# Performance work log

Measured on AMD Instinct MI355X. Metric: run time of the kernel, lower is better.

Reference implementation:

```python
import jax, jax.numpy as jnp
import numpy as np

D_MODEL = 1024
N_HEADS = 16
HEAD_DIM = 64
T = 4096
ROT = HEAD_DIM // 2          # 32 channels get rotary
PAIR = ROT // 2              # 16 cos/sin frequencies
EPS = 1e-6
SCALE = 0.12                 # constant attention scale (not 1/sqrt(d))
ROPE_BASE = 10000.0
VOCAB = 50257


def setup_inputs() -> dict:
    key = jax.random.key(0)
    k_x, k_qkv, k_o, k_tok = jax.random.split(key, 4)
    bound = 0.5 / np.sqrt(D_MODEL)
    x = jax.random.normal(k_x, (1, T, D_MODEL), dtype=jnp.float32)
    w_qkv = jax.random.uniform(k_qkv, (3 * D_MODEL, D_MODEL), jnp.float32, -bound, bound)
    # module uses zero_init for w_o; use small random so output is non-trivial
    w_o = jax.random.uniform(k_o, (D_MODEL, D_MODEL), jnp.float32, -bound, bound)
    q_norm_w = jnp.ones((HEAD_DIM,), jnp.float32)
    k_norm_w = jnp.ones((HEAD_DIM,), jnp.float32)
    tokens = jax.random.randint(k_tok, (1, T), 0, VOCAB, dtype=jnp.int64)
    pos = jnp.arange(T, dtype=jnp.int64)
    # RotaryCache: inv_freq over pair dims, cos/sin of t * inv_freq
    inv_freq = 1.0 / (ROPE_BASE ** (jnp.arange(PAIR, dtype=jnp.float32) / PAIR))
    freqs = jnp.arange(T, dtype=jnp.float32)[:, None] * inv_freq[None, :]  # [T, PAIR]
    return {
        "x": x, "tokens": tokens, "pos": pos,
        "w_qkv": w_qkv, "w_o": w_o,
        "q_norm_w": q_norm_w, "k_norm_w": k_norm_w,
        "cos": jnp.cos(freqs), "sin": jnp.sin(freqs),
        "window_tokens": 1024, "block_size": 128,
    }


def _rmsnorm(x, w):
    var = jnp.mean(x * x, axis=-1, keepdims=True)
    return x * jax.lax.rsqrt(var + EPS) * w


def reference(x, tokens, pos, w_qkv, w_o, q_norm_w, k_norm_w, cos, sin,
              window_tokens, block_size):
    B, Tq, C = x.shape
    H, Dh = N_HEADS, HEAD_DIM
    qkv = x @ w_qkv.T                                  # [B, T, 3C]
    q, k, v = jnp.split(qkv, 3, axis=-1)

    def to_bhtd(t):
        return t.reshape(B, Tq, H, Dh).transpose(0, 2, 1, 3)
    q, k, v = to_bhtd(q), to_bhtd(k), to_bhtd(v)

    q = _rmsnorm(q, q_norm_w)
    k = _rmsnorm(k, k_norm_w)

    # half-truncated RoPE: rotate first ROT channels pairwise (even/odd)
    c = cos[pos][None, None]                           # [1,1,T,PAIR]
    s = sin[pos][None, None]

    def rope_rotate(t):
        t1, t2 = t[..., :ROT], t[..., ROT:]
        even, odd = t1[..., 0::2], t1[..., 1::2]
        r_even = even * c - odd * s
        r_odd = even * s + odd * c
        t1r = jnp.stack([r_even, r_odd], axis=-1).reshape(t1.shape)
        return jnp.concatenate([t1r, t2], axis=-1)

    q = rope_rotate(q)
    k = rope_rotate(k)

    v = v * 0.5                                        # no value-embed branch

    scores = jnp.einsum('bhtd,bhsd->bhts', q, k) * SCALE
    idx = jnp.arange(Tq)
    diff = idx[:, None] - idx[None, :]
    allowed = (diff >= 0) & (diff < window_tokens)     # sliding causal window
    scores = jnp.where(allowed, scores, -jnp.inf)
    p = jax.nn.softmax(scores, axis=-1)
    out = jnp.einsum('bhts,bhsd->bhtd', p, v)
    out = out.transpose(0, 2, 1, 3).reshape(B, Tq, C)
    return out @ w_o.T
```

## Files before the change

### kernel.cpp

```cpp
#include <hip/hip_runtime.h>


typedef __bf16 bf16x8 __attribute__((ext_vector_type(8)));
typedef __bf16 bf16x2 __attribute__((ext_vector_type(2)));
typedef float f32x4 __attribute__((ext_vector_type(4)));
typedef unsigned short u16x8 __attribute__((ext_vector_type(8)));
typedef unsigned short u16x4 __attribute__((ext_vector_type(4)));

#define MFMA16(a, b, c) __builtin_amdgcn_mfma_f32_16x16x32_bf16((a), (b), (c), 0, 0, 0)

__device__ __forceinline__ unsigned short f2bf(float f) {
    unsigned int u = __float_as_uint(f);
    u += 0x7fffu + ((u >> 16) & 1u);
    return (unsigned short)(u >> 16);
}
__device__ __forceinline__ float bf2f(unsigned short h) {
    return __uint_as_float(((unsigned int)h) << 16);
}
__device__ __forceinline__ unsigned int pk2bf(float a, float b) {
#if __has_builtin(__builtin_amdgcn_cvt_pk_bf16_f32)
    bf16x2 v = __builtin_amdgcn_cvt_pk_bf16_f32(a, b);
    return __builtin_bit_cast(unsigned int, v);
#else
    return (unsigned int)f2bf(a) | ((unsigned int)f2bf(b) << 16);
#endif
}
__device__ __forceinline__ float fexp2(float x) {
#if __has_builtin(__builtin_amdgcn_exp2f)
    return __builtin_amdgcn_exp2f(x);
#else
    return exp2f(x);
#endif
}

__device__ __forceinline__ void gl_lds16(const void* g, void* l) {
    typedef __attribute__((address_space(1))) unsigned int GU;
    typedef __attribute__((address_space(3))) unsigned int LU;
    __builtin_amdgcn_global_load_lds((GU*)(unsigned long long)g,
                                     (LU*)(unsigned int)(unsigned long long)l,
                                     16, 0, 0);
}

__global__ void cvt3_kernel(const float* __restrict__ x,
                            const float* __restrict__ wqkv,
                            const float* __restrict__ wo,
                            unsigned short* __restrict__ xb,
                            unsigned short* __restrict__ wqkvb,
                            unsigned short* __restrict__ wob) {
    int i = blockIdx.x * 256 + threadIdx.x;
    const float* src;
    unsigned short* dst;
    int off;
    if (i < 1048576) { src = x; dst = xb; off = i; }
    else if (i < 1835008) { src = wqkv; dst = wqkvb; off = i - 1048576; }
    else { src = wo; dst = wob; off = i - 1835008; }
    float4 f = ((const float4*)src)[off];
    u16x4 o;
    o[0] = f2bf(f.x); o[1] = f2bf(f.y); o[2] = f2bf(f.z); o[3] = f2bf(f.w);
    ((u16x4*)dst)[off] = o;
}

#define TBS 72
__global__ __launch_bounds__(256, 3) void gemm_qkv(
    const unsigned short* __restrict__ A,
    const unsigned short* __restrict__ Bt,
    const float* __restrict__ cosb, const float* __restrict__ sinb,
    const float* __restrict__ qw, const float* __restrict__ kw,
    unsigned short* __restrict__ Qb,
    unsigned short* __restrict__ Kb,
    unsigned short* __restrict__ Vt)
{
    __shared__ unsigned short smem[16384];
    unsigned short* As0 = smem;
    unsigned short* As1 = smem + 4096;
    unsigned short* Bs0 = smem + 8192;
    unsigned short* Bs1 = smem + 12288;

    const int tid = threadIdx.x;
    const int wave = tid >> 6, lane = tid & 63;
    const int quad = lane >> 4, l16 = lane & 15;
    const int m0 = blockIdx.x * 128, n0 = blockIdx.y * 128;
    const int wm = (wave >> 1) * 64, wn = (wave & 1) * 64;

    f32x4 acc[4][4];
#pragma unroll
    for (int i = 0; i < 4; ++i)
#pragma unroll
        for (int j = 0; j < 4; ++j) acc[i][j] = (f32x4){0.f, 0.f, 0.f, 0.f};

    const int lrow = lane >> 2;
    const int lcol = ((lane & 3) ^ ((lane >> 3) & 3)) * 8;
    const int csw  = (quad ^ ((l16 >> 1) & 3)) * 8;

    for (int k0 = 0; k0 < 1024; k0 += 64) {
        {
            const unsigned short* ab = A + (size_t)(m0 + wave * 16 + lrow) * 1024 + k0 + lcol;
            gl_lds16(ab,              &As0[wave * 512]);
            gl_lds16(ab + 32,         &As1[wave * 512]);
            gl_lds16(ab + 65536,      &As0[2048 + wave * 512]);
            gl_lds16(ab + 65536 + 32, &As1[2048 + wave * 512]);
            const unsigned short* bb = Bt + (size_t)(n0 + wave * 16 + lrow) * 1024 + k0 + lcol;
            gl_lds16(bb,              &Bs0[wave * 512]);
            gl_lds16(bb + 32,         &Bs1[wave * 512]);
            gl_lds16(bb + 65536,      &Bs0[2048 + wave * 512]);
            gl_lds16(bb + 65536 + 32, &Bs1[2048 + wave * 512]);
        }
        __syncthreads();
        {
            bf16x8 af[4], bfr[4];
#pragma unroll
            for (int mt = 0; mt < 4; ++mt)
                af[mt] = *(const bf16x8*)&As0[(wm + mt * 16 + l16) * 32 + csw];
#pragma unroll
            for (int nt = 0; nt < 4; ++nt)
                bfr[nt] = *(const bf16x8*)&Bs0[(wn + nt * 16 + l16) * 32 + csw];
#pragma unroll
            for (int mt = 0; mt < 4; ++mt)
#pragma unroll
                for (int nt = 0; nt < 4; ++nt)
                    acc[mt][nt] = MFMA16(af[mt], bfr[nt], acc[mt][nt]);
        }
        {
            bf16x8 af[4], bfr[4];
#pragma unroll
            for (int mt = 0; mt < 4; ++mt)
                af[mt] = *(const bf16x8*)&As1[(wm + mt * 16 + l16) * 32 + csw];
#pragma unroll
            for (int nt = 0; nt < 4; ++nt)
                bfr[nt] = *(const bf16x8*)&Bs1[(wn + nt * 16 + l16) * 32 + csw];
#pragma unroll
            for (int mt = 0; mt < 4; ++mt)
#pragma unroll
                for (int nt = 0; nt < 4; ++nt)
                    acc[mt][nt] = MFMA16(af[mt], bfr[nt], acc[mt][nt]);
        }
        __syncthreads();
    }

    unsigned short* tbw = smem + wave * 1152;
    const int region = blockIdx.y >> 3;
    const int h = ((blockIdx.y & 7) << 1) + (wave & 1);

    if (region < 2) {
        const float* wgt = region ? kw : qw;
        unsigned short* dst = region ? Kb : Qb;
        const float post = region ? 1.f : 0.17312340490667046f;
        float w[4];
#pragma unroll
        for (int nt = 0; nt < 4; ++nt) w[nt] = wgt[nt * 16 + l16] * post;
#pragma unroll
        for (int mt = 0; mt < 4; ++mt) {
#pragma unroll
            for (int r = 0; r < 4; ++r) {
                const int row = m0 + wm + mt * 16 + quad * 4 + r;
                float ss = 0.f;
#pragma unroll
                for (int nt = 0; nt < 4; ++nt)
                    ss += acc[mt][nt][r] * acc[mt][nt][r];
                ss += __shfl_xor(ss, 1); ss += __shfl_xor(ss, 2);
                ss += __shfl_xor(ss, 4); ss += __shfl_xor(ss, 8);
                const float rn = rsqrtf(ss * (1.f / 64.f) + 1e-6f);
                float val[4];
#pragma unroll
                for (int nt = 0; nt < 4; ++nt)
                    val[nt] = acc[mt][nt][r] * rn * w[nt];
#pragma unroll
                for (int nt = 0; nt < 2; ++nt) {
                    const float prt = __shfl_xor(val[nt], 1);
                    const int p = nt * 8 + (l16 >> 1);
                    const float c = cosb[row * 16 + p];
                    const float s = sinb[row * 16 + p];
                    val[nt] = (l16 & 1) ? (prt * s + val[nt] * c)
                                        : (val[nt] * c - prt * s);
                }
#pragma unroll
                for (int nt = 0; nt < 4; ++nt)
                    tbw[(quad * 4 + r) * TBS + nt * 16 + l16] = f2bf(val[nt]);
            }
            const int t = lane >> 2, dcol = (lane & 3) * 16;
            u16x8 v0 = *(const u16x8*)&tbw[t * TBS + dcol];
            u16x8 v1 = *(const u16x8*)&tbw[t * TBS + dcol + 8];
            const size_t ob = ((size_t)h * 4096 + (m0 + wm + mt * 16 + t)) * 64 + dcol;
            *(u16x8*)&dst[ob] = v0;
            *(u16x8*)&dst[ob + 8] = v1;
        }
    } else {
#pragma unroll
        for (int mt = 0; mt < 4; ++mt) {
#pragma unroll
            for (int nt = 0; nt < 4; ++nt)
#pragma unroll
                for (int r = 0; r < 4; ++r)
                    tbw[(nt * 16 + l16) * 16 + quad * 4 + r] =
                        f2bf(acc[mt][nt][r] * 0.5f);
            u16x8 v0 = *(const u16x8*)&tbw[lane * 16];
            u16x8 v1 = *(const u16x8*)&tbw[lane * 16 + 8];
            const size_t vo = ((size_t)h * 64 + lane) * 4096 + m0 + wm + mt * 16;
            *(u16x8*)&Vt[vo] = v0;
            *(u16x8*)&Vt[vo + 8] = v1;
        }
    }
}

#define PSTR 72

template <int MASK>
__device__ __forceinline__ void attn_compute(
    int s0, int tq, int quad, int l16, int csw,
    const unsigned short* Ks0, const unsigned short* Ks1,
    const unsigned short* Vs0, const unsigned short* Vs1,
    unsigned short* Pw, const bf16x8 qf0, const bf16x8 qf1,
    f32x4 (&o)[4], float& lsum)
{
#pragma unroll
    for (int i = 0; i < 4; ++i) {
        const bf16x8 kf0 = *(const bf16x8*)&Ks0[(i * 16 + l16) * 32 + csw];
        const bf16x8 kf1 = *(const bf16x8*)&Ks1[(i * 16 + l16) * 32 + csw];
        f32x4 z = (f32x4){0.f, 0.f, 0.f, 0.f};
        z = MFMA16(kf0, qf0, z);
        z = MFMA16(kf1, qf1, z);
        float p[4];
#pragma unroll
        for (int r = 0; r < 4; ++r) {
            float e = fexp2(z[r]);
            if (MASK) {
                const int s = s0 + i * 16 + quad * 4 + r;
                e = ((unsigned)(tq - s) < 1024u) ? e : 0.f;
            }
            p[r] = e;
            lsum += e;
        }
        uint2 pk;
        pk.x = pk2bf(p[0], p[1]);
        pk.y = pk2bf(p[2], p[3]);
        *(uint2*)&Pw[l16 * PSTR + i * 16 + quad * 4] = pk;
    }
    const bf16x8 pf0 = *(const bf16x8*)&Pw[l16 * PSTR + quad * 8];
    const bf16x8 pf1 = *(const bf16x8*)&Pw[l16 * PSTR + 32 + quad * 8];
#pragma unroll
    for (int dt = 0; dt < 4; ++dt) {
        const bf16x8 vf0 = *(const bf16x8*)&Vs0[(dt * 16 + l16) * 32 + csw];
        const bf16x8 vf1 = *(const bf16x8*)&Vs1[(dt * 16 + l16) * 32 + csw];
        o[dt] = MFMA16(pf0, vf0, o[dt]);
        o[dt] = MFMA16(pf1, vf1, o[dt]);
    }
}

__global__ __launch_bounds__(512, 4) void attn_kernel(
    const unsigned short* __restrict__ Qb,
    const unsigned short* __restrict__ Kb,
    const unsigned short* __restrict__ Vt,
    unsigned short* __restrict__ att)
{
    __shared__ unsigned short Ks0[2][2048], Ks1[2][2048];
    __shared__ unsigned short Vs0[2][2048], Vs1[2][2048];
    __shared__ unsigned short P[8][16 * PSTR];

    const int bid = blockIdx.x;
    const int h = ((bid & 7) << 1) | ((bid >> 3) & 1);
    const int t0 = (31 - (bid >> 4)) * 128;

    const int tid = threadIdx.x;
    const int wave = tid >> 6, lane = tid & 63;
    const int quad = lane >> 4, l16 = lane & 15;
    const int qt0 = t0 + wave * 16;
    const int tq = qt0 + l16;
    const int srow = (tid & 255) >> 2;
    const int scol = ((tid & 3) ^ ((tid >> 3) & 3)) * 8;
    const int csw  = (quad ^ ((l16 >> 1) & 3)) * 8;

    const unsigned short* Qh = Qb + (size_t)h * 4096 * 64;
    const unsigned short* Kh = Kb + (size_t)h * 4096 * 64;
    const unsigned short* Vh = Vt + (size_t)h * 64 * 4096;

    const bf16x8 qf0 = *(const bf16x8*)&Qh[(qt0 + l16) * 64 + quad * 8];
    const bf16x8 qf1 = *(const bf16x8*)&Qh[(qt0 + l16) * 64 + 32 + quad * 8];

    f32x4 o[4];
#pragma unroll
    for (int dt = 0; dt < 4; ++dt) o[dt] = (f32x4){0.f, 0.f, 0.f, 0.f};
    float lsum = 0.f;
    unsigned short* Pw = P[wave];

    auto stage = [&](int b, int s0) {
        if (wave < 4) {
            const unsigned short* kb = Kh + (size_t)(s0 + srow) * 64 + scol;
            gl_lds16(kb,      &Ks0[b][wave * 512]);
            gl_lds16(kb + 32, &Ks1[b][wave * 512]);
        } else {
            const unsigned short* vb = Vh + (size_t)srow * 4096 + s0 + scol;
            gl_lds16(vb,      &Vs0[b][(wave - 4) * 512]);
            gl_lds16(vb + 32, &Vs1[b][(wave - 4) * 512]);
        }
    };

    const int s_lo = (t0 >= 1024) ? (t0 - 1024) : 0;
    const int s_hi = t0 + 64;
    stage(0, s_lo);
    __syncthreads();
    int buf = 0;
    for (int s0 = s_lo; s0 <= s_hi; s0 += 64) {
        if (s0 < s_hi) stage(buf ^ 1, s0 + 64);
        const bool dead = (s0 > qt0 + 15) || (s0 + 63 < qt0 - 1023);
        if (!dead) {
            const bool clean = (s0 + 63 <= qt0) && (s0 >= qt0 - 1008);
            if (clean)
                attn_compute<0>(s0, tq, quad, l16, csw, Ks0[buf], Ks1[buf],
                                Vs0[buf], Vs1[buf], Pw, qf0, qf1, o, lsum);
            else
                attn_compute<1>(s0, tq, quad, l16, csw, Ks0[buf], Ks1[buf],
                                Vs0[buf], Vs1[buf], Pw, qf0, qf1, o, lsum);
        }
        __syncthreads();
        buf ^= 1;
    }

    lsum += __shfl_xor(lsum, 16);
    lsum += __shfl_xor(lsum, 32);
    float lr[4];
#pragma unroll
    for (int r = 0; r < 4; ++r) lr[r] = 1.f / __shfl(lsum, quad * 4 + r);
#pragma unroll
    for (int dt = 0; dt < 4; ++dt)
#pragma unroll
        for (int r = 0; r < 4; ++r)
            att[(size_t)(qt0 + quad * 4 + r) * 1024 + h * 64 + dt * 16 + l16] =
                f2bf(o[dt][r] * lr[r]);
}

__global__ __launch_bounds__(256) void gemm_out(
    const unsigned short* __restrict__ A,
    const unsigned short* __restrict__ Bt,
    float* __restrict__ C)
{
    __shared__ unsigned short As0[2][2048], As1[2][2048];
    __shared__ unsigned short Bs0[2][4096], Bs1[2][4096];
    const int tid = threadIdx.x;
    const int wave = tid >> 6, lane = tid & 63;
    const int quad = lane >> 4, l16 = lane & 15;
    const int m0 = blockIdx.x * 64, n0 = blockIdx.y * 128;
    const int wm = (wave >> 1) * 32, wn = (wave & 1) * 64;
    const int lrow = lane >> 2;
    const int lcol = ((lane & 3) ^ ((lane >> 3) & 3)) * 8;
    const int csw  = (quad ^ ((l16 >> 1) & 3)) * 8;

    f32x4 acc[2][4];
#pragma unroll
    for (int i = 0; i < 2; ++i)
#pragma unroll
        for (int j = 0; j < 4; ++j) acc[i][j] = (f32x4){0.f, 0.f, 0.f, 0.f};

    auto stage = [&](int buf, int k0) {
        const unsigned short* ab = A + (size_t)(m0 + wave * 16 + lrow) * 1024 + k0 + lcol;
        gl_lds16(ab,      &As0[buf][wave * 512]);
        gl_lds16(ab + 32, &As1[buf][wave * 512]);
#pragma unroll
        for (int i = 0; i < 2; ++i) {
            const int c = wave * 2 + i;
            const unsigned short* bb = Bt + (size_t)(n0 + c * 16 + lrow) * 1024 + k0 + lcol;
            gl_lds16(bb,      &Bs0[buf][c * 512]);
            gl_lds16(bb + 32, &Bs1[buf][c * 512]);
        }
    };

    stage(0, 0);
    __syncthreads();
    int buf = 0;
    for (int k0 = 0; k0 < 1024; k0 += 64) {
        if (k0 + 64 < 1024) stage(buf ^ 1, k0 + 64);
        {
            bf16x8 af[2], bfr[4];
#pragma unroll
            for (int mt = 0; mt < 2; ++mt)
                af[mt] = *(const bf16x8*)&As0[buf][(wm + mt * 16 + l16) * 32 + csw];
#pragma unroll
            for (int nt = 0; nt < 4; ++nt)
                bfr[nt] = *(const bf16x8*)&Bs0[buf][(wn + nt * 16 + l16) * 32 + csw];
#pragma unroll
            for (int mt = 0; mt < 2; ++mt)
#pragma unroll
                for (int nt = 0; nt < 4; ++nt)
                    acc[mt][nt] = MFMA16(af[mt], bfr[nt], acc[mt][nt]);
        }
        {
            bf16x8 af[2], bfr[4];
#pragma unroll
            for (int mt = 0; mt < 2; ++mt)
                af[mt] = *(const bf16x8*)&As1[buf][(wm + mt * 16 + l16) * 32 + csw];
#pragma unroll
            for (int nt = 0; nt < 4; ++nt)
                bfr[nt] = *(const bf16x8*)&Bs1[buf][(wn + nt * 16 + l16) * 32 + csw];
#pragma unroll
            for (int mt = 0; mt < 2; ++mt)
#pragma unroll
                for (int nt = 0; nt < 4; ++nt)
                    acc[mt][nt] = MFMA16(af[mt], bfr[nt], acc[mt][nt]);
        }
        __syncthreads();
        buf ^= 1;
    }
#pragma unroll
    for (int mt = 0; mt < 2; ++mt)
#pragma unroll
        for (int nt = 0; nt < 4; ++nt)
#pragma unroll
            for (int r = 0; r < 4; ++r) {
                const int row = m0 + wm + mt * 16 + quad * 4 + r;
                const int col = n0 + wn + nt * 16 + l16;
                C[(size_t)row * 1024 + col] = acc[mt][nt][r];
            }
}

extern "C" void kernel_launch(void* const* d_in, const int* in_sizes, int n_in,
                              void* d_out, int out_size, void* d_ws, size_t ws_size,
                              hipStream_t stream) {
    const float* x    = (const float*)d_in[0];
    const float* wqkv = (const float*)d_in[3];
    const float* wo   = (const float*)d_in[4];
    const float* qw   = (const float*)d_in[5];
    const float* kw   = (const float*)d_in[6];
    const float* cosb = (const float*)d_in[7];
    const float* sinb = (const float*)d_in[8];

    char* ws = (char*)d_ws;
    if (ws_size < (size_t)48 * 1024 * 1024) return;
    unsigned short* xb    = (unsigned short*)(ws + ((size_t)0 << 20));
    unsigned short* wqkvb = (unsigned short*)(ws + ((size_t)8 << 20));
    unsigned short* wob   = (unsigned short*)(ws + ((size_t)14 << 20));
    unsigned short* Qb    = (unsigned short*)(ws + ((size_t)16 << 20));
    unsigned short* Kb    = (unsigned short*)(ws + ((size_t)24 << 20));
    unsigned short* Vt    = (unsigned short*)(ws + ((size_t)32 << 20));
    unsigned short* attb  = (unsigned short*)(ws + ((size_t)40 << 20));

    cvt3_kernel<<<8192, 256, 0, stream>>>(x, wqkv, wo, xb, wqkvb, wob);

    gemm_qkv<<<dim3(32, 24), 256, 0, stream>>>(xb, wqkvb, cosb, sinb, qw, kw,
                                               Qb, Kb, Vt);

    attn_kernel<<<512, 512, 0, stream>>>(Qb, Kb, Vt, attb);

    gemm_out<<<dim3(64, 8), 256, 0, stream>>>(attb, wob, (float*)d_out);
}
```

Before: 177.9 us.

## Restructure attention loop into 128-key tiles with split K/V staging and setprio

The attention main loop now processes 128 keys per iteration as two 64-key halves. K tiles are double-buffered one iteration ahead, while V is single-buffered and loaded within the same iteration, overlapping with the first QK/exp pass before a mid-iteration barrier. The PV MFMA section is wrapped in s_setprio to favour matrix issue. This halves the number of loop iterations and barriers per key, but V load latency is now exposed inside each iteration and LDS use goes up.

```diff
diff --git a/kernel.cpp b/kernel.cpp
--- a/kernel.cpp
+++ b/kernel.cpp
@@ -205,17 +205,15 @@
 #define PSTR 72
 
 template <int MASK>
-__device__ __forceinline__ void attn_compute(
-    int s0, int tq, int quad, int l16, int csw,
-    const unsigned short* Ks0, const unsigned short* Ks1,
-    const unsigned short* Vs0, const unsigned short* Vs1,
-    unsigned short* Pw, const bf16x8 qf0, const bf16x8 qf1,
-    f32x4 (&o)[4], float& lsum)
+__device__ __forceinline__ void qk_exp(
+    int sb, int tq, int quad, int l16, int csw, int rbase,
+    const unsigned short* KsA, const unsigned short* KsB,
+    unsigned short* Pw, const bf16x8 qf0, const bf16x8 qf1, float& lsum)
 {
 #pragma unroll
     for (int i = 0; i < 4; ++i) {
-        const bf16x8 kf0 = *(const bf16x8*)&Ks0[(i * 16 + l16) * 32 + csw];
-        const bf16x8 kf1 = *(const bf16x8*)&Ks1[(i * 16 + l16) * 32 + csw];
+        const bf16x8 kf0 = *(const bf16x8*)&KsA[(rbase + i * 16 + l16) * 32 + csw];
+        const bf16x8 kf1 = *(const bf16x8*)&KsB[(rbase + i * 16 + l16) * 32 + csw];
         f32x4 z = (f32x4){0.f, 0.f, 0.f, 0.f};
         z = MFMA16(kf0, qf0, z);
         z = MFMA16(kf1, qf1, z);
@@ -224,7 +222,7 @@
         for (int r = 0; r < 4; ++r) {
             float e = fexp2(z[r]);
             if (MASK) {
-                const int s = s0 + i * 16 + quad * 4 + r;
+                const int s = sb + i * 16 + quad * 4 + r;
                 e = ((unsigned)(tq - s) < 1024u) ? e : 0.f;
             }
             p[r] = e;
@@ -235,15 +233,24 @@
         pk.y = pk2bf(p[2], p[3]);
         *(uint2*)&Pw[l16 * PSTR + i * 16 + quad * 4] = pk;
     }
+}
+
+__device__ __forceinline__ void pv_acc(
+    int quad, int l16, int csw,
+    const unsigned short* VsA, const unsigned short* VsB,
+    const unsigned short* Pw, f32x4 (&o)[4])
+{
     const bf16x8 pf0 = *(const bf16x8*)&Pw[l16 * PSTR + quad * 8];
     const bf16x8 pf1 = *(const bf16x8*)&Pw[l16 * PSTR + 32 + quad * 8];
+    __builtin_amdgcn_s_setprio(1);
 #pragma unroll
     for (int dt = 0; dt < 4; ++dt) {
-        const bf16x8 vf0 = *(const bf16x8*)&Vs0[(dt * 16 + l16) * 32 + csw];
-        const bf16x8 vf1 = *(const bf16x8*)&Vs1[(dt * 16 + l16) * 32 + csw];
+        const bf16x8 vf0 = *(const bf16x8*)&VsA[(dt * 16 + l16) * 32 + csw];
+        const bf16x8 vf1 = *(const bf16x8*)&VsB[(dt * 16 + l16) * 32 + csw];
         o[dt] = MFMA16(pf0, vf0, o[dt]);
         o[dt] = MFMA16(pf1, vf1, o[dt]);
     }
+    __builtin_amdgcn_s_setprio(0);
 }
 
 __global__ __launch_bounds__(512, 4) void attn_kernel(
@@ -252,8 +259,9 @@
     const unsigned short* __restrict__ Vt,
     unsigned short* __restrict__ att)
 {
-    __shared__ unsigned short Ks0[2][2048], Ks1[2][2048];
-    __shared__ unsigned short Vs0[2][2048], Vs1[2][2048];
+    __shared__ unsigned short KsA[2][4096], KsB[2][4096];
+    __shared__ unsigned short Vs0[2048], Vs1[2048];
+    __shared__ unsigned short Vs2[2048], Vs3[2048];
     __shared__ unsigned short P[8][16 * PSTR];
 
     const int bid = blockIdx.x;
@@ -282,34 +290,54 @@
     float lsum = 0.f;
     unsigned short* Pw = P[wave];
 
-    auto stage = [&](int b, int s0) {
+    auto stageK = [&](int b, int s) {
         if (wave < 4) {
-            const unsigned short* kb = Kh + (size_t)(s0 + srow) * 64 + scol;
-            gl_lds16(kb,      &Ks0[b][wave * 512]);
-            gl_lds16(kb + 32, &Ks1[b][wave * 512]);
-        } else {
-            const unsigned short* vb = Vh + (size_t)srow * 4096 + s0 + scol;
-            gl_lds16(vb,      &Vs0[b][(wave - 4) * 512]);
-            gl_lds16(vb + 32, &Vs1[b][(wave - 4) * 512]);
+            const unsigned short* kb = Kh + (size_t)(s + srow) * 64 + scol;
+            gl_lds16(kb,             &KsA[b][wave * 512]);
+            gl_lds16(kb + 32,        &KsB[b][wave * 512]);
+            gl_lds16(kb + 4096,      &KsA[b][2048 + wave * 512]);
+            gl_lds16(kb + 4096 + 32, &KsB[b][2048 + wave * 512]);
         }
     };
+    auto stageV = [&](int s) {
+        if (wave >= 4) {
+            const unsigned short* vb = Vh + (size_t)srow * 4096 + s + scol;
+            gl_lds16(vb,      &Vs0[(wave - 4) * 512]);
+            gl_lds16(vb + 32, &Vs1[(wave - 4) * 512]);
+            gl_lds16(vb + 64, &Vs2[(wave - 4) * 512]);
+            gl_lds16(vb + 96, &Vs3[(wave - 4) * 512]);
+        }
+    };
 
     const int s_lo = (t0 >= 1024) ? (t0 - 1024) : 0;
-    const int s_hi = t0 + 64;
-    stage(0, s_lo);
+    const int NT = ((t0 - s_lo) >> 7) + 1;
+
+    stageK(0, s_lo);
     __syncthreads();
     int buf = 0;
-    for (int s0 = s_lo; s0 <= s_hi; s0 += 64) {
-        if (s0 < s_hi) stage(buf ^ 1, s0 + 64);
-        const bool dead = (s0 > qt0 + 15) || (s0 + 63 < qt0 - 1023);
-        if (!dead) {
-            const bool clean = (s0 + 63 <= qt0) && (s0 >= qt0 - 1008);
-            if (clean)
-                attn_compute<0>(s0, tq, quad, l16, csw, Ks0[buf], Ks1[buf],
-                                Vs0[buf], Vs1[buf], Pw, qf0, qf1, o, lsum);
-            else
-                attn_compute<1>(s0, tq, quad, l16, csw, Ks0[buf], Ks1[buf],
-                                Vs0[buf], Vs1[buf], Pw, qf0, qf1, o, lsum);
+    for (int n = 0; n < NT; ++n) {
+        const int s0 = s_lo + n * 128;
+        const int sb1 = s0 + 64;
+        if (n + 1 < NT) stageK(buf ^ 1, s0 + 128);
+        stageV(s0);
+        const bool d0 = (s0 + 63 < qt0 - 1023);
+        const bool c0 = (s0 + 63 <= qt0) && (s0 >= qt0 - 1008);
+        const bool d1 = (sb1 > qt0 + 15) || (sb1 + 63 < qt0 - 1023);
+        const bool c1 = (sb1 + 63 <= qt0) && (sb1 >= qt0 - 1008);
+        if (!d0) {
+            if (c0) qk_exp<0>(s0, tq, quad, l16, csw, 0, KsA[buf], KsB[buf],
+                              Pw, qf0, qf1, lsum);
+            else    qk_exp<1>(s0, tq, quad, l16, csw, 0, KsA[buf], KsB[buf],
+                              Pw, qf0, qf1, lsum);
+        }
+        __syncthreads();
+        if (!d0) pv_acc(quad, l16, csw, Vs0, Vs1, Pw, o);
+        if (!d1) {
+            if (c1) qk_exp<0>(sb1, tq, quad, l16, csw, 64, KsA[buf], KsB[buf],
+                              Pw, qf0, qf1, lsum);
+            else    qk_exp<1>(sb1, tq, quad, l16, csw, 64, KsA[buf], KsB[buf],
+                              Pw, qf0, qf1, lsum);
+            pv_acc(quad, l16, csw, Vs2, Vs3, Pw, o);
         }
         __syncthreads();
         buf ^= 1;
```

Result: no change. 177.1 us (-0.5%).
